# Kernel optimization log

Hardware: AMD Instinct MI355X
Metric: run time of the kernel (lower is better)

## Reference

```python
import jax, jax.numpy as jnp
import numpy as np

K = 3  # kernel_size
P = 1  # padding (must satisfy K == 2*P+1 for the original einsum to be shape-valid)


def setup_inputs() -> dict:
    key = jax.random.key(0)
    k1, k2, k3 = jax.random.split(key, 3)
    b, i, c, L, o = 16, 64, 4, 4096, 64
    x = jax.random.normal(k1, (b, i, c, L), dtype=jnp.float32)
    time_tensor = jax.random.uniform(k2, (b, c, L), dtype=jnp.float32)
    weights = jax.random.normal(k3, (o, i, c, K), dtype=jnp.float32)
    return {"x": x, "time_tensor": time_tensor, "weights": weights}


def reference(x, time_tensor, weights):
    """x: (b,i,c,L), time_tensor: (b,c,L), weights: (o,i,c,K) -> (b,o,c,L).

    Faithful to the torch module: pad x/time by P on the time axis, unfold x
    into sliding windows, pad the unfolded tensor again by P, multiply by the
    time scalar per (b,c,l) and contract over (i,k), then crop P from each end.
    The time factor is scalar per output element, so we factor it out of the
    einsum instead of materializing the (b,o,i,c,k,l) dynamic_weights tensor --
    mathematically identical, massively cheaper.
    """
    xp = jnp.pad(x, ((0, 0), (0, 0), (0, 0), (P, P)))            # (b,i,c,L+2P)
    tp = jnp.pad(time_tensor, ((0, 0), (0, 0), (P, P)))          # (b,c,L+2P)
    Lw = xp.shape[-1] - K + 1                                    # == L since K=2P+1
    # unfold -> (b,i,c,K,Lw), matching torch's permute(0,2,1,4,3) after transpose
    xu = jnp.stack([xp[..., j:j + Lw] for j in range(K)], axis=-2)
    xu = jnp.transpose(xu, (0, 2, 1, 3, 4))                      # (b,c,i,K,Lw)
    xu = jnp.pad(xu, ((0, 0), (0, 0), (0, 0), (0, 0), (P, P)))   # (b,c,i,K,Lw+2P)
    conv = jnp.einsum('oick,bcikl->bocl', weights, xu)           # (b,o,c,L+2P)
    out = conv * tp[:, None, :, :]
    return out[..., P:-P]                                        # (b,o,c,L)
```

## Files before the change

kernel.cpp:

```cpp
#include <hip/hip_runtime.h>


#define NB 16
#define NI 64
#define NC 4
#define NL 4096
#define NO 64
#define KW 3
#define LT 32
#define NCH 8
#define LBLK (LT * NCH)
#define ROWS (LBLK + 2)
#define ROWB 128
#define LDSB (ROWS * ROWB)

#define W_PACK_BYTES (NO * NI * NC * KW * 2)

typedef float f32x4 __attribute__((ext_vector_type(4)));
typedef short bf16x8 __attribute__((ext_vector_type(8)));

__device__ inline unsigned short f2bf(float f) {
    unsigned int u = __builtin_bit_cast(unsigned int, f);
    u += 0x7FFFu + ((u >> 16) & 1u);
    return (unsigned short)(u >> 16);
}

__device__ __forceinline__ void block_sync_lds() {
    asm volatile("s_waitcnt lgkmcnt(0)" ::: "memory");
    __builtin_amdgcn_s_barrier();
    asm volatile("" ::: "memory");
}

__global__ __launch_bounds__(256)
void prepack_w_kernel(const float* __restrict__ w, unsigned short* __restrict__ wp) {
    const int idx = blockIdx.x * 256 + threadIdx.x;
    const float v = w[idx];
    const int k = idx % 3;
    int r = idx / 3;
    const int c = r & 3;  r >>= 2;
    const int i = r & 63;
    const int o = r >> 6;
    const int cc   = k * 2 + (i >> 5);
    const int lane = (((i >> 3) & 3) << 4) | (o & 15);
    const int j    = i & 7;
    const int wv   = o >> 4;
    wp[(((c * 4 + wv) * 6 + cc) * 64 + lane) * 8 + j] = f2bf(v);
}

__device__ __forceinline__ void stage_load(const float* __restrict__ xb,
                                           int l0q, int g2, f32x4 s[2]) {
    const float* p = xb + (size_t)(2 * g2) * (NC * NL) + l0q;
    s[0] = *(const f32x4*)(p);
    s[1] = *(const f32x4*)(p + NC * NL);
}

__device__ __forceinline__ void stage_write(char* __restrict__ lds,
                                            int ch, int q, int g2,
                                            const f32x4 s[2]) {
#pragma unroll
    for (int r = 0; r < 4; ++r) {
        const int row = ch * LT + 4 * q + r + 1;
        const unsigned int pk =
            (unsigned int)f2bf(s[0][r]) | ((unsigned int)f2bf(s[1][r]) << 16);
        *(unsigned int*)(lds + row * ROWB + ((4 * g2) ^ ((row & 7) << 4))) = pk;
    }
}

__device__ __forceinline__ void compute_chunk(const char* __restrict__ lds,
                                              const bf16x8 wfrag[2][6],
                                              const float* __restrict__ tb,
                                              float* __restrict__ ob0,
                                              float* __restrict__ ob1,
                                              int ch, int lb0, int lane, int lh) {
    const int lcol  = lane & 15;
    const int ksub2 = (lane >> 4) * 16;
    const int l0 = lb0 + ch * LT + lh * 16 + (lane >> 4) * 4;
    const f32x4 tv = *(const f32x4*)(tb + l0);

    f32x4 acc0 = {}, acc1 = {};
#pragma unroll
    for (int cc = 0; cc < 6; ++cc) {
        const int row = ch * LT + lh * 16 + lcol + (cc >> 1);
        const int off = row * ROWB + ((((cc & 1) << 6) + ksub2) ^ ((row & 7) << 4));
        const bf16x8 xf = *(const bf16x8*)(lds + off);
        acc0 = __builtin_amdgcn_mfma_f32_16x16x32_bf16(xf, wfrag[0][cc], acc0, 0, 0, 0);
        acc1 = __builtin_amdgcn_mfma_f32_16x16x32_bf16(xf, wfrag[1][cc], acc1, 0, 0, 0);
    }
    f32x4 r0, r1;
#pragma unroll
    for (int qq = 0; qq < 4; ++qq) { r0[qq] = acc0[qq] * tv[qq]; r1[qq] = acc1[qq] * tv[qq]; }
    *(f32x4*)(ob0 + l0) = r0;
    *(f32x4*)(ob1 + l0) = r1;
}

__global__ __launch_bounds__(256, 4)
void tconv_mfma_kernel(const float* __restrict__ x,
                       const float* __restrict__ tt,
                       const unsigned short* __restrict__ wp,
                       float* __restrict__ out)
{
    __shared__ char lds[LDSB];

    const int t    = threadIdx.x;
    const int lane = t & 63;
    const int wave = t >> 6;
    const int oh   = wave >> 1;
    const int lh   = wave & 1;
    const int c    = blockIdx.y;
    const int b    = blockIdx.z;
    const int lb0  = blockIdx.x * LBLK;
    const int g2   = t >> 3;
    const int q    = t & 7;
    const int lq   = 4 * q;

    const float* xb = x + ((size_t)b * NI * NC + c) * NL;
    const float* tb = tt + (size_t)(b * NC + c) * NL;
    float* ob0 = out + ((size_t)b * NO * NC
                        + (size_t)(oh * 32 + (lane & 15)) * NC + c) * NL;
    float* ob1 = ob0 + (size_t)16 * NC * NL;

    f32x4 sA[2], sB[2];
    stage_load(xb, lb0 + 0 * LT + lq, g2, sA);
    stage_load(xb, lb0 + 1 * LT + lq, g2, sB);
    float h = 0.f; int hrow = 0, hcol = 0;
    if (t < 128) {
        const int which = t & 1;
        const int i     = t >> 1;
        hrow = which ? (LBLK + 1) : 0;
        hcol = 2 * i;
        const int lhh = which ? (lb0 + LBLK) : (lb0 - 1);
        if (lhh >= 0 && lhh < NL) h = xb[(size_t)i * (NC * NL) + lhh];
    }

    bf16x8 wfrag[2][6];
    {
        const bf16x8* wpb = (const bf16x8*)wp + (size_t)((c * 4 + oh * 2) * 6) * 64 + lane;
#pragma unroll
        for (int s = 0; s < 2; ++s)
#pragma unroll
            for (int cc = 0; cc < 6; ++cc)
                wfrag[s][cc] = wpb[(s * 6 + cc) * 64];
    }

    stage_write(lds, 0, q, g2, sA);
    stage_write(lds, 1, q, g2, sB);
    if (t < 128)
        *(unsigned short*)(lds + hrow * ROWB + (hcol ^ ((hrow & 7) << 4))) = f2bf(h);
    block_sync_lds();

#pragma unroll
    for (int cn = 0; cn < NCH - 2; ++cn) {
        if ((cn & 1) == 0) {
            stage_load(xb, lb0 + (cn + 2) * LT + lq, g2, sA);
            compute_chunk(lds, wfrag, tb, ob0, ob1, cn, lb0, lane, lh);
            stage_write(lds, cn + 2, q, g2, sA);
        } else {
            stage_load(xb, lb0 + (cn + 2) * LT + lq, g2, sB);
            compute_chunk(lds, wfrag, tb, ob0, ob1, cn, lb0, lane, lh);
            stage_write(lds, cn + 2, q, g2, sB);
        }
        block_sync_lds();
    }

    compute_chunk(lds, wfrag, tb, ob0, ob1, NCH - 2, lb0, lane, lh);
    compute_chunk(lds, wfrag, tb, ob0, ob1, NCH - 1, lb0, lane, lh);
}

extern "C" void kernel_launch(void* const* d_in, const int* in_sizes, int n_in,
                              void* d_out, int out_size, void* d_ws, size_t ws_size,
                              hipStream_t stream) {
    const float* x  = (const float*)d_in[0];
    const float* tt = (const float*)d_in[1];
    const float* w  = (const float*)d_in[2];
    float* out = (float*)d_out;
    unsigned short* wpck = (unsigned short*)d_ws;

    prepack_w_kernel<<<dim3(NO * NI * NC * KW / 256), dim3(256), 0, stream>>>(w, wpck);

    dim3 grid(NL / LBLK, NC, NB);
    tconv_mfma_kernel<<<grid, dim3(256), 0, stream>>>(x, tt, wpck, out);
}
```

Before: 33.46 us.

## Split producer and consumer waves and double the chunk length

Each block now runs 8 waves. Four producer waves load x from global memory, convert it to bf16 and write it to LDS. Four consumer waves hold the weight fragments and run the MFMA compute plus the time-scale stores, staying in lockstep with the producers through matching barrier counts. LT doubles, so each block covers 512 positions and the grid is halved. The goal is to overlap global loads with MFMA work. The cost is a larger LDS buffer (~65KB per block), fewer blocks to hide latency, and half the waves not doing compute on a kernel that is largely bandwidth-bound.

```diff
diff --git a/kernel.cpp b/kernel.cpp
--- a/kernel.cpp
+++ b/kernel.cpp
@@ -7,7 +7,7 @@
 #define NL 4096
 #define NO 64
 #define KW 3
-#define LT 32
+#define LT 64
 #define NCH 8
 #define LBLK (LT * NCH)
 #define ROWS (LBLK + 2)
@@ -18,6 +18,7 @@
 
 typedef float f32x4 __attribute__((ext_vector_type(4)));
 typedef short bf16x8 __attribute__((ext_vector_type(8)));
+typedef unsigned int u32x2 __attribute__((ext_vector_type(2)));
 
 __device__ inline unsigned short f2bf(float f) {
     unsigned int u = __builtin_bit_cast(unsigned int, f);
@@ -48,21 +49,23 @@
 }
 
 __device__ __forceinline__ void stage_load(const float* __restrict__ xb,
-                                           int l0q, int g2, f32x4 s[2]) {
-    const float* p = xb + (size_t)(2 * g2) * (NC * NL) + l0q;
+                                           int l0, int g, f32x4 s[4]) {
+    const float* p = xb + (size_t)(4 * g) * (NC * NL) + l0;
     s[0] = *(const f32x4*)(p);
     s[1] = *(const f32x4*)(p + NC * NL);
+    s[2] = *(const f32x4*)(p + 2 * NC * NL);
+    s[3] = *(const f32x4*)(p + 3 * NC * NL);
 }
 
 __device__ __forceinline__ void stage_write(char* __restrict__ lds,
-                                            int ch, int q, int g2,
-                                            const f32x4 s[2]) {
+                                            int r0, int g, const f32x4 s[4]) {
 #pragma unroll
     for (int r = 0; r < 4; ++r) {
-        const int row = ch * LT + 4 * q + r + 1;
-        const unsigned int pk =
-            (unsigned int)f2bf(s[0][r]) | ((unsigned int)f2bf(s[1][r]) << 16);
-        *(unsigned int*)(lds + row * ROWB + ((4 * g2) ^ ((row & 7) << 4))) = pk;
+        const int rr = r0 + r;
+        u32x2 pk;
+        pk[0] = (unsigned int)f2bf(s[0][r]) | ((unsigned int)f2bf(s[1][r]) << 16);
+        pk[1] = (unsigned int)f2bf(s[2][r]) | ((unsigned int)f2bf(s[3][r]) << 16);
+        *(u32x2*)(lds + rr * ROWB + ((8 * g) ^ ((rr & 7) << 4))) = pk;
     }
 }
 
@@ -71,29 +74,33 @@
                                               const float* __restrict__ tb,
                                               float* __restrict__ ob0,
                                               float* __restrict__ ob1,
-                                              int ch, int lb0, int lane, int lh) {
+                                              int ch, int lb0, int lane, int lhp) {
     const int lcol  = lane & 15;
     const int ksub2 = (lane >> 4) * 16;
-    const int l0 = lb0 + ch * LT + lh * 16 + (lane >> 4) * 4;
-    const f32x4 tv = *(const f32x4*)(tb + l0);
-
-    f32x4 acc0 = {}, acc1 = {};
 #pragma unroll
-    for (int cc = 0; cc < 6; ++cc) {
-        const int row = ch * LT + lh * 16 + lcol + (cc >> 1);
-        const int off = row * ROWB + ((((cc & 1) << 6) + ksub2) ^ ((row & 7) << 4));
-        const bf16x8 xf = *(const bf16x8*)(lds + off);
-        acc0 = __builtin_amdgcn_mfma_f32_16x16x32_bf16(xf, wfrag[0][cc], acc0, 0, 0, 0);
-        acc1 = __builtin_amdgcn_mfma_f32_16x16x32_bf16(xf, wfrag[1][cc], acc1, 0, 0, 0);
+    for (int lt2 = 0; lt2 < 2; ++lt2) {
+        const int sub  = lhp * 2 + lt2;
+        const int base = ch * LT + sub * 16;
+        const int l0   = lb0 + base + (lane >> 4) * 4;
+        const f32x4 tv = *(const f32x4*)(tb + l0);
+        f32x4 acc0 = {}, acc1 = {};
+#pragma unroll
+        for (int cc = 0; cc < 6; ++cc) {
+            const int row = base + lcol + (cc >> 1);
+            const int off = row * ROWB + ((((cc & 1) << 6) + ksub2) ^ ((row & 7) << 4));
+            const bf16x8 xf = *(const bf16x8*)(lds + off);
+            acc0 = __builtin_amdgcn_mfma_f32_16x16x32_bf16(xf, wfrag[0][cc], acc0, 0, 0, 0);
+            acc1 = __builtin_amdgcn_mfma_f32_16x16x32_bf16(xf, wfrag[1][cc], acc1, 0, 0, 0);
+        }
+        f32x4 r0, r1;
+#pragma unroll
+        for (int q = 0; q < 4; ++q) { r0[q] = acc0[q] * tv[q]; r1[q] = acc1[q] * tv[q]; }
+        *(f32x4*)(ob0 + l0) = r0;
+        *(f32x4*)(ob1 + l0) = r1;
     }
-    f32x4 r0, r1;
-#pragma unroll
-    for (int qq = 0; qq < 4; ++qq) { r0[qq] = acc0[qq] * tv[qq]; r1[qq] = acc1[qq] * tv[qq]; }
-    *(f32x4*)(ob0 + l0) = r0;
-    *(f32x4*)(ob1 + l0) = r1;
 }
 
-__global__ __launch_bounds__(256, 4)
+__global__ __launch_bounds__(512, 4)
 void tconv_mfma_kernel(const float* __restrict__ x,
                        const float* __restrict__ tt,
                        const unsigned short* __restrict__ wp,
@@ -104,66 +111,75 @@
     const int t    = threadIdx.x;
     const int lane = t & 63;
     const int wave = t >> 6;
-    const int oh   = wave >> 1;
-    const int lh   = wave & 1;
     const int c    = blockIdx.y;
     const int b    = blockIdx.z;
     const int lb0  = blockIdx.x * LBLK;
-    const int g2   = t >> 3;
-    const int q    = t & 7;
-    const int lq   = 4 * q;
 
     const float* xb = x + ((size_t)b * NI * NC + c) * NL;
-    const float* tb = tt + (size_t)(b * NC + c) * NL;
-    float* ob0 = out + ((size_t)b * NO * NC
-                        + (size_t)(oh * 32 + (lane & 15)) * NC + c) * NL;
-    float* ob1 = ob0 + (size_t)16 * NC * NL;
 
-    f32x4 sA[2], sB[2];
-    stage_load(xb, lb0 + 0 * LT + lq, g2, sA);
-    stage_load(xb, lb0 + 1 * LT + lq, g2, sB);
-    float h = 0.f; int hrow = 0, hcol = 0;
-    if (t < 128) {
-        const int which = t & 1;
-        const int i     = t >> 1;
-        hrow = which ? (LBLK + 1) : 0;
-        hcol = 2 * i;
-        const int lhh = which ? (lb0 + LBLK) : (lb0 - 1);
-        if (lhh >= 0 && lhh < NL) h = xb[(size_t)i * (NC * NL) + lhh];
-    }
+    if (wave < 4) {
+        const int g  = t >> 4;
+        const int lq = 4 * (t & 15);
 
-    bf16x8 wfrag[2][6];
-    {
-        const bf16x8* wpb = (const bf16x8*)wp + (size_t)((c * 4 + oh * 2) * 6) * 64 + lane;
-#pragma unroll
-        for (int s = 0; s < 2; ++s)
-#pragma unroll
-            for (int cc = 0; cc < 6; ++cc)
-                wfrag[s][cc] = wpb[(s * 6 + cc) * 64];
-    }
-
-    stage_write(lds, 0, q, g2, sA);
-    stage_write(lds, 1, q, g2, sB);
-    if (t < 128)
-        *(unsigned short*)(lds + hrow * ROWB + (hcol ^ ((hrow & 7) << 4))) = f2bf(h);
-    block_sync_lds();
+        f32x4 sA[4], sB[4];
+        stage_load(xb, lb0 + 0 * LT + lq, g, sA);
+        stage_load(xb, lb0 + 1 * LT + lq, g, sB);
+        float h = 0.f; int hrow = 0, hcol = 0;
+        if (t < 128) {
+            const int which = t & 1;
+            const int i     = t >> 1;
+            hrow = which ? (LBLK + 1) : 0;
+            hcol = 2 * i;
+            const int lh = which ? (lb0 + LBLK) : (lb0 - 1);
+            if (lh >= 0 && lh < NL) h = xb[(size_t)i * (NC * NL) + lh];
+        }
+        stage_write(lds, 1 + 0 * LT + lq, g, sA);
+        stage_write(lds, 1 + 1 * LT + lq, g, sB);
+        if (t < 128)
+            *(unsigned short*)(lds + hrow * ROWB + (hcol ^ ((hrow & 7) << 4))) = f2bf(h);
+        block_sync_lds();
 
 #pragma unroll
-    for (int cn = 0; cn < NCH - 2; ++cn) {
-        if ((cn & 1) == 0) {
-            stage_load(xb, lb0 + (cn + 2) * LT + lq, g2, sA);
-            compute_chunk(lds, wfrag, tb, ob0, ob1, cn, lb0, lane, lh);
-            stage_write(lds, cn + 2, q, g2, sA);
-        } else {
-            stage_load(xb, lb0 + (cn + 2) * LT + lq, g2, sB);
-            compute_chunk(lds, wfrag, tb, ob0, ob1, cn, lb0, lane, lh);
-            stage_write(lds, cn + 2, q, g2, sB);
+        for (int cn = 0; cn < NCH - 2; ++cn) {
+            if ((cn & 1) == 0) {
+                stage_load(xb, lb0 + (cn + 2) * LT + lq, g, sA);
+                stage_write(lds, 1 + (cn + 2) * LT + lq, g, sA);
+            } else {
+                stage_load(xb, lb0 + (cn + 2) * LT + lq, g, sB);
+                stage_write(lds, 1 + (cn + 2) * LT + lq, g, sB);
+            }
+            block_sync_lds();
         }
+    } else {
+        const int cw  = wave - 4;
+        const int oh  = cw >> 1;
+        const int lhp = cw & 1;
+
+        bf16x8 wfrag[2][6];
+        {
+            const bf16x8* wpb = (const bf16x8*)wp
+                + (size_t)((c * 4 + 2 * oh) * 6) * 64 + lane;
+#pragma unroll
+            for (int s = 0; s < 2; ++s)
+#pragma unroll
+                for (int cc = 0; cc < 6; ++cc)
+                    wfrag[s][cc] = wpb[(s * 6 + cc) * 64];
+        }
+        const float* tb = tt + (size_t)(b * NC + c) * NL;
+        float* ob0 = out + ((size_t)b * NO * NC
+                            + (size_t)(oh * 32 + (lane & 15)) * NC + c) * NL;
+        float* ob1 = ob0 + (size_t)16 * NC * NL;
+
         block_sync_lds();
+
+#pragma unroll
+        for (int cn = 0; cn < NCH - 2; ++cn) {
+            compute_chunk(lds, wfrag, tb, ob0, ob1, cn, lb0, lane, lhp);
+            block_sync_lds();
+        }
+        compute_chunk(lds, wfrag, tb, ob0, ob1, NCH - 2, lb0, lane, lhp);
+        compute_chunk(lds, wfrag, tb, ob0, ob1, NCH - 1, lb0, lane, lhp);
     }
-
-    compute_chunk(lds, wfrag, tb, ob0, ob1, NCH - 2, lb0, lane, lh);
-    compute_chunk(lds, wfrag, tb, ob0, ob1, NCH - 1, lb0, lane, lh);
 }
 
 extern "C" void kernel_launch(void* const* d_in, const int* in_sizes, int n_in,
@@ -178,5 +194,5 @@
     prepack_w_kernel<<<dim3(NO * NI * NC * KW / 256), dim3(256), 0, stream>>>(w, wpck);
 
     dim3 grid(NL / LBLK, NC, NB);
-    tconv_mfma_kernel<<<grid, dim3(256), 0, stream>>>(x, tt, wpck, out);
+    tconv_mfma_kernel<<<grid, dim3(512), 0, stream>>>(x, tt, wpck, out);
 }
```

Measured after the change: 32.77 us. 1.02x faster.
